# Kernel tuning notes

Measured on AMD Instinct MI355X. Metric: run time of the kernel, lower is better.

Reference implementation:

```python
import jax, jax.numpy as jnp
import numpy as np

L, H, NH, B, S = 6, 768, 12, 4, 1024
D = H // NH
SCALE = 1.0 / np.sqrt(D)
EPS = 1e-5


def setup_inputs() -> dict:
    key = jax.random.key(0)
    ks = jax.random.split(key, 20)
    std = np.sqrt(2.0 / (5.0 * H)).astype(np.float32)
    w = lambda k, shape: (jax.random.normal(k, shape, jnp.float32) * std)
    x = jax.random.normal(ks[0], (B, S, H), jnp.float32)
    lengths = jnp.array([1024, 896, 768, 640])  # no fully-masked rows
    pad_mask = jnp.arange(S)[None, :] >= lengths[:, None]  # True = padding
    inp = {
        "x": x,
        "pad_mask": pad_mask,
        "Wq": w(ks[1], (L, H, H)), "bq": jnp.zeros((L, H), jnp.float32),
        "Wk": w(ks[2], (L, H, H)), "bk": w(ks[3], (L, H)) * 0.1,
        "Wv": w(ks[4], (L, H, H)), "bv": w(ks[5], (L, H)) * 0.1,
        "Wo": w(ks[6], (L, H, H)), "bo": jnp.zeros((L, H), jnp.float32),
        "ln1_g": jnp.ones((L, H), jnp.float32), "ln1_b": jnp.zeros((L, H), jnp.float32),
        "ln2_g": jnp.ones((L, H), jnp.float32), "ln2_b": jnp.zeros((L, H), jnp.float32),
        "W1": w(ks[7], (L, 8 * H, H)), "b1": jnp.zeros((L, 8 * H), jnp.float32),
        "W2": w(ks[8], (L, H, 4 * H)), "b2": jnp.zeros((L, H), jnp.float32),
        "out_g": jnp.ones((H,), jnp.float32), "out_b": jnp.zeros((H,), jnp.float32),
    }
    return inp


def _ln(x, g, b):
    m = jnp.mean(x, axis=-1, keepdims=True)
    v = jnp.mean(jnp.square(x - m), axis=-1, keepdims=True)
    return (x - m) * jax.lax.rsqrt(v + EPS) * g + b


def _encoder(x, pad_mask, params):
    def layer(x, p):
        (Wq, bq, Wk, bk, Wv, bv, Wo, bo, g1, be1, g2, be2, W1, b1, W2, b2) = p
        Bz, Sl, Hd = x.shape
        xn = _ln(x, g1, be1)
        q = (xn @ Wq.T + bq).reshape(Bz, Sl, NH, D)
        k = (xn @ Wk.T + bk).reshape(Bz, Sl, NH, D)
        v = (xn @ Wv.T + bv).reshape(Bz, Sl, NH, D)
        scores = jnp.einsum('bqhd,bkhd->bhqk', q, k) * SCALE
        scores = jnp.where(pad_mask[:, None, None, :], -jnp.inf, scores)
        probs = jax.nn.softmax(scores, axis=-1)
        av = jnp.einsum('bhqk,bkhd->bqhd', probs, v).reshape(Bz, Sl, Hd)
        x = x + (av @ Wo.T + bo)
        xn = _ln(x, g2, be2)
        h = xn @ W1.T + b1
        u, gate = jnp.split(h, 2, axis=-1)
        x = x + (u * jax.nn.gelu(gate, approximate=False)) @ W2.T + b2
        return x, None

    x, _ = jax.lax.scan(layer, x, params)
    return x


def reference(x, pad_mask, Wq, bq, Wk, bk, Wv, bv, Wo, bo,
              ln1_g, ln1_b, ln2_g, ln2_b, W1, b1, W2, b2, out_g, out_b):
    params = (Wq, bq, Wk, bk, Wv, bv, Wo, bo,
              ln1_g, ln1_b, ln2_g, ln2_b, W1, b1, W2, b2)
    x = _encoder(x, pad_mask, params)
    return _ln(x, out_g, out_b)
```

## Files before the change

kernel.cpp:

```cpp
#include <hip/hip_runtime.h>

typedef unsigned short u16;
typedef __bf16 bf16x8 __attribute__((ext_vector_type(8)));
typedef unsigned short us8 __attribute__((ext_vector_type(8)));
typedef unsigned short us4 __attribute__((ext_vector_type(4)));
typedef float f32x4 __attribute__((ext_vector_type(4)));

typedef __attribute__((address_space(3))) unsigned int as3_uint;
typedef const __attribute__((address_space(1))) unsigned int as1_cuint;

__device__ __forceinline__ u16 f2bf(float f) {
    unsigned u = __float_as_uint(f);
    u += 0x7FFFu + ((u >> 16) & 1u);
    return (u16)(u >> 16);
}
__device__ __forceinline__ float bf2f(u16 h) {
    return __uint_as_float(((unsigned)h) << 16);
}
__device__ __forceinline__ bf16x8 ld8(const u16* p) {
    return __builtin_bit_cast(bf16x8, *(const us8*)p);
}
#define MFMA16(a, b, c) __builtin_amdgcn_mfma_f32_16x16x32_bf16(a, b, c, 0, 0, 0)

__device__ __forceinline__ void glds16(const void* g, void* l) {
    __builtin_amdgcn_global_load_lds((as1_cuint*)g, (as3_uint*)l, 16, 0, 0);
}

__global__ void detect_k(const unsigned* __restrict__ pm, int* __restrict__ len4) {
    __shared__ int isbool;
    const int t = threadIdx.x;
    if (t == 0) isbool = 0;
    __syncthreads();
    unsigned orv = pm[t] | pm[256 + t] | pm[512 + t] | pm[768 + t];
    if (orv & 0xFFFFFF00u) atomicOr(&isbool, 1);
    __syncthreads();
    const int w = t >> 6, l = t & 63;
    int cnt = 0;
    if (isbool) {
        const unsigned char* p8 = (const unsigned char*)pm;
        for (int i = l; i < 1024; i += 64) cnt += (p8[w * 1024 + i] == 0) ? 1 : 0;
    } else {
        for (int i = l; i < 1024; i += 64) cnt += (pm[w * 1024 + i] == 0u) ? 1 : 0;
    }
#pragma unroll
    for (int m = 1; m < 64; m <<= 1) cnt += __shfl_xor(cnt, m);
    if (l == 0) {
        int c = cnt;
        if (c < 1) c = 1;
        if (c > 1024) c = 1024;
        len4[w] = c;
    }
}

__global__ __launch_bounds__(256) void conv_k(
    const float* __restrict__ Wq, const float* __restrict__ Wk,
    const float* __restrict__ Wv, const float* __restrict__ Wo,
    const float* __restrict__ W1, const float* __restrict__ W2,
    const float* __restrict__ bq, const float* __restrict__ bk,
    const float* __restrict__ bv,
    u16* __restrict__ wqkvo, u16* __restrict__ w1b, u16* __restrict__ w2b,
    float* __restrict__ bqkv, int lyr) {
    const int idx = blockIdx.x * 256 + threadIdx.x;
    const size_t e = (size_t)idx * 4;
    const float* src;
    u16* dst;
    if (e < 2359296u) {
        int which = (int)(e / 589824u);
        size_t off = e % 589824u;
        const float* m = (which == 0) ? Wq : (which == 1) ? Wk : (which == 2) ? Wv : Wo;
        src = m + (size_t)lyr * 589824u + off;
        dst = wqkvo + e;
    } else if (e < 7077888u) {
        size_t off = e - 2359296u;
        src = W1 + (size_t)lyr * 4718592u + off;
        dst = w1b + off;
    } else {
        size_t off = e - 7077888u;
        src = W2 + (size_t)lyr * 2359296u + off;
        dst = w2b + off;
    }
    float4 v = *(const float4*)src;
    us4 o;
    o[0] = f2bf(v.x); o[1] = f2bf(v.y); o[2] = f2bf(v.z); o[3] = f2bf(v.w);
    *(us4*)dst = o;
    if (idx < 2304) {
        float bb = (idx < 768) ? bq[lyr * 768 + idx]
                 : (idx < 1536) ? bk[lyr * 768 + idx - 768]
                                : bv[lyr * 768 + idx - 1536];
        bqkv[idx] = bb;
    }
}

template <int OUTF>
__global__ __launch_bounds__(256) void ln_k(const float* __restrict__ x,
                                            const float* __restrict__ gm,
                                            const float* __restrict__ bt,
                                            void* __restrict__ outp) {
    const int w = threadIdx.x >> 6, l = threadIdx.x & 63;
    const int row = blockIdx.x * 4 + w;
    const float4* xr = (const float4*)(x + (size_t)row * 768);
    float4 v[3];
    float s = 0.f, ss = 0.f;
#pragma unroll
    for (int i = 0; i < 3; ++i) {
        v[i] = xr[i * 64 + l];
        s += v[i].x + v[i].y + v[i].z + v[i].w;
        ss += v[i].x * v[i].x + v[i].y * v[i].y + v[i].z * v[i].z + v[i].w * v[i].w;
    }
#pragma unroll
    for (int m = 1; m < 64; m <<= 1) {
        s += __shfl_xor(s, m);
        ss += __shfl_xor(ss, m);
    }
    const float mean = s * (1.f / 768.f);
    float var = ss * (1.f / 768.f) - mean * mean;
    var = fmaxf(var, 0.f);
    const float rs = rsqrtf(var + 1e-5f);
    const float4* g4 = (const float4*)gm;
    const float4* b4 = (const float4*)bt;
#pragma unroll
    for (int i = 0; i < 3; ++i) {
        float4 gg = g4[i * 64 + l], bb = b4[i * 64 + l];
        float o0 = (v[i].x - mean) * rs * gg.x + bb.x;
        float o1 = (v[i].y - mean) * rs * gg.y + bb.y;
        float o2 = (v[i].z - mean) * rs * gg.z + bb.z;
        float o3 = (v[i].w - mean) * rs * gg.w + bb.w;
        if (OUTF) {
            ((float4*)outp)[(size_t)row * 192 + i * 64 + l] = make_float4(o0, o1, o2, o3);
        } else {
            us4 pk;
            pk[0] = f2bf(o0); pk[1] = f2bf(o1); pk[2] = f2bf(o2); pk[3] = f2bf(o3);
            ((us4*)outp)[(size_t)row * 192 + i * 64 + l] = pk;
        }
    }
}

template <int VAR>
__global__ __launch_bounds__(512, 2) void gemm256_k(
    const u16* __restrict__ A, const u16* __restrict__ W,
    const float* __restrict__ bias, u16* __restrict__ outp, int ldout) {
    __shared__ __align__(16) u16 lds[2][4][8192];
    const int tid = threadIdx.x;
    const int w = tid >> 6, l = tid & 63, ax = l & 15, gx = l >> 4;
    const int wr = w >> 2, wc = w & 3;
    const int nwg = gridDim.x;
    const int bid = blockIdx.x;
    const int swz = (bid & 7) * (nwg >> 3) + (bid >> 3);
    const int nb = swz >> 4, mb = swz & 15;
    const int m0 = mb * 256;
    const int K = 768;

    const int row0 = tid >> 2, cc0 = (tid & 3) ^ ((row0 >> 1) & 3);
    const int row1 = 128 + row0, cc1 = (tid & 3) ^ ((row1 >> 1) & 3);
    const size_t goA0 = (size_t)row0 * K + cc0 * 8;
    const size_t goA1 = (size_t)row1 * K + cc1 * 8;
    const u16* Ab = A + (size_t)m0 * K;
    const u16* Bb0;
    const u16* Bb1;
    if constexpr (VAR == 0) {
        Bb0 = W + (size_t)(nb * 256) * K;
        Bb1 = Bb0;
    } else {
        Bb0 = W + (size_t)(nb * 128) * K;
        Bb1 = W + (size_t)(3072 + nb * 128 - 128) * K;
    }

    auto stage = [&](int u, int kt) {
        const int kh = u & 1;
        const size_t koff = (size_t)kt * 64 + kh * 32;
        u16* d = (u16*)&lds[kt & 1][u][0];
        if (u < 2) {
            glds16(Ab + goA0 + koff, d + tid * 8);
            glds16(Ab + goA1 + koff, d + (512 + tid) * 8);
        } else {
            glds16(Bb0 + goA0 + koff, d + tid * 8);
            glds16(Bb1 + goA1 + koff, d + (512 + tid) * 8);
        }
    };

    bf16x8 rav[4], rbv[4];
    f32x4 acc[8][4] = {};

    auto phase = [&](int buf, int q, int kh, int readB, int vm, int su, int skt) {
        if (vm == 8) asm volatile("s_waitcnt vmcnt(8)" ::: "memory");
        else if (vm == 4) asm volatile("s_waitcnt vmcnt(4)" ::: "memory");
        else if (vm == 0) asm volatile("s_waitcnt vmcnt(0)" ::: "memory");
        __builtin_amdgcn_s_barrier();
        if (readB) {
#pragma unroll
            for (int j = 0; j < 4; ++j) {
                int row = (VAR == 0) ? (wc * 64 + j * 16 + ax)
                                     : ((j >> 1) * 128 + wc * 32 + (j & 1) * 16 + ax);
                rbv[j] = ld8(&lds[buf][2 + kh][row * 32 + ((gx ^ ((row >> 1) & 3)) * 8)]);
            }
        }
#pragma unroll
        for (int mf = 0; mf < 4; ++mf) {
            int row = wr * 128 + q * 64 + mf * 16 + ax;
            rav[mf] = ld8(&lds[buf][kh][row * 32 + ((gx ^ ((row >> 1) & 3)) * 8)]);
        }
        if (su >= 0) stage(su, skt);
        asm volatile("s_waitcnt lgkmcnt(0)" ::: "memory");
        __builtin_amdgcn_sched_barrier(0);
        __builtin_amdgcn_s_setprio(1);
#pragma unroll
        for (int mf = 0; mf < 4; ++mf)
#pragma unroll
            for (int j = 0; j < 4; ++j)
                acc[q * 4 + mf][j] = MFMA16(rav[mf], rbv[j], acc[q * 4 + mf][j]);
        __builtin_amdgcn_s_setprio(0);
    };

    stage(0, 0); stage(2, 0); stage(1, 0); stage(3, 0); stage(0, 1); stage(2, 1);

#pragma unroll 1
    for (int t = 0; t < 5; ++t) {
        const int O = 2 * t + 1, E2 = 2 * t + 2, O2 = 2 * t + 3;
        phase(0, 0, 0, 1, 8, 1, O);
        phase(0, 1, 0, 0, -1, 3, O);
        phase(0, 0, 1, 1, 8, 0, E2);
        phase(0, 1, 1, 0, -1, 2, E2);
        phase(1, 0, 0, 1, 8, 1, E2);
        phase(1, 1, 0, 0, -1, 3, E2);
        phase(1, 0, 1, 1, 8, 0, O2);
        phase(1, 1, 1, 0, -1, 2, O2);
    }
    phase(0, 0, 0, 1, 8, 1, 11);
    phase(0, 1, 0, 0, -1, 3, 11);
    phase(0, 0, 1, 1, 8, -1, 0);
    phase(0, 1, 1, 0, -1, -1, 0);
    phase(1, 0, 0, 1, 4, -1, 0);
    phase(1, 1, 0, 0, -1, -1, 0);
    phase(1, 0, 1, 1, 0, -1, 0);
    phase(1, 1, 1, 0, -1, -1, 0);

    const int rowb = m0 + wr * 128;
    if constexpr (VAR == 0) {
#pragma unroll
        for (int j = 0; j < 4; ++j) {
            const int col = nb * 256 + wc * 64 + j * 16 + ax;
            const float bn = bias[col];
#pragma unroll
            for (int am = 0; am < 8; ++am) {
                const int rb_ = rowb + am * 16 + 4 * gx;
#pragma unroll
                for (int r = 0; r < 4; ++r)
                    outp[(size_t)(rb_ + r) * ldout + col] = f2bf(acc[am][j][r] + bn);
            }
        }
    } else {
#pragma unroll
        for (int nf = 0; nf < 2; ++nf) {
            const int col = nb * 128 + wc * 32 + nf * 16 + ax;
            const float bu_ = bias[col], bg_ = bias[3072 + col];
#pragma unroll
            for (int am = 0; am < 8; ++am) {
                const int rb_ = rowb + am * 16 + 4 * gx;
#pragma unroll
                for (int r = 0; r < 4; ++r) {
                    float uu = acc[am][nf][r] + bu_;
                    float gg = acc[am][2 + nf][r] + bg_;
                    float gel = 0.5f * gg * (1.f + erff(gg * 0.70710678118f));
                    outp[(size_t)(rb_ + r) * ldout + col] = f2bf(uu * gel);
                }
            }
        }
    }
}

template <int EPI>
__global__ __launch_bounds__(256) void gemm_k(
    const u16* __restrict__ A, const u16* __restrict__ W,
    const float* __restrict__ bias, const float* __restrict__ resid,
    void* __restrict__ outp, int N, int K) {
    __shared__ __align__(16) u16 As[2][128 * 64];
    __shared__ __align__(16) u16 Bs[2][128 * 64];
    const int tid = threadIdx.x;
    const int w = tid >> 6, l = tid & 63, a = l & 15, g = l >> 4;
    const int wr = w >> 1, wc = w & 1;
    const int m0 = blockIdx.y * 128, n0 = blockIdx.x * 128;
    f32x4 acc[4][4] = {};
    const int nk = K >> 6;

    auto stage = [&](int kt, int buf) {
        const int k0 = kt * 64;
#pragma unroll
        for (int i = 0; i < 4; ++i) {
            int c = i * 256 + tid;
            int row = c >> 3, cc = c & 7, c8 = cc ^ (row & 7);
            glds16(A + (size_t)(m0 + row) * K + k0 + c8 * 8, &As[buf][c * 8]);
        }
#pragma unroll
        for (int i = 0; i < 4; ++i) {
            int c = i * 256 + tid;
            int row = c >> 3, cc = c & 7, c8 = cc ^ (row & 7);
            glds16(W + (size_t)(n0 + row) * K + k0 + c8 * 8, &Bs[buf][c * 8]);
        }
    };

    stage(0, 0);
    int cur = 0;
    for (int kt = 0; kt < nk; ++kt) {
        if (kt + 1 < nk) {
            stage(kt + 1, cur ^ 1);
            __builtin_amdgcn_sched_barrier(0);
            asm volatile("s_waitcnt vmcnt(8)" ::: "memory");
        } else {
            __builtin_amdgcn_sched_barrier(0);
            asm volatile("s_waitcnt vmcnt(0)" ::: "memory");
        }
        __builtin_amdgcn_s_barrier();
#pragma unroll
        for (int ks = 0; ks < 2; ++ks) {
            bf16x8 af[4], bv_[4];
#pragma unroll
            for (int m = 0; m < 4; ++m) {
                int row = wr * 64 + m * 16 + a;
                af[m] = ld8(&As[cur][row * 64 + (((ks * 4 + g) ^ (a & 7)) * 8)]);
            }
#pragma unroll
            for (int n = 0; n < 4; ++n) {
                int row = wc * 64 + n * 16 + a;
                bv_[n] = ld8(&Bs[cur][row * 64 + (((ks * 4 + g) ^ (a & 7)) * 8)]);
            }
#pragma unroll
            for (int m = 0; m < 4; ++m)
#pragma unroll
                for (int n = 0; n < 4; ++n)
                    acc[m][n] = MFMA16(af[m], bv_[n], acc[m][n]);
        }
        __builtin_amdgcn_s_barrier();
        cur ^= 1;
    }
    u16* outu = (u16*)outp;
    float* outf = (float*)outp;
    const int row0 = m0 + wr * 64, col0 = n0 + wc * 64;
#pragma unroll
    for (int n = 0; n < 4; ++n) {
        const int col = col0 + n * 16 + a;
        const float bn = bias[col];
#pragma unroll
        for (int m = 0; m < 4; ++m) {
            const int rb = row0 + m * 16 + 4 * g;
#pragma unroll
            for (int r = 0; r < 4; ++r) {
                const size_t off = (size_t)(rb + r) * N + col;
                float vv = acc[m][n][r] + bn;
                if constexpr (EPI == 0) {
                    outu[off] = f2bf(vv);
                } else {
                    outf[off] = vv + resid[off];
                }
            }
        }
    }
}

__global__ __launch_bounds__(256) void attn_k(const u16* __restrict__ qkv,
                                              u16* __restrict__ av,
                                              const int* __restrict__ len4) {
    __shared__ __align__(16) u16 Ks[64 * 64];
    __shared__ __align__(16) u16 Vt[64 * 64];
    __shared__ __align__(16) u16 Ps[4][16 * 64];
    const int tid = threadIdx.x;
    const int w = tid >> 6, l = tid & 63, a = l & 15, g = l >> 4;
    const int qb = blockIdx.x, h = blockIdx.y, b = blockIdx.z;
    const size_t rowQ = (size_t)(b * 1024 + qb * 64 + w * 16 + a);
    const u16* qp = qkv + rowQ * 2304 + h * 64;
    bf16x8 qf[2];
    qf[0] = __builtin_bit_cast(bf16x8, *(const us8*)(qp + g * 8));
    qf[1] = __builtin_bit_cast(bf16x8, *(const us8*)(qp + 32 + g * 8));
    f32x4 O[4] = {};
    float m_r[4], l_r[4];
#pragma unroll
    for (int r = 0; r < 4; ++r) { m_r[r] = -1e30f; l_r[r] = 0.f; }
    const int length = len4[b];
    const int nkt = (length + 63) >> 6;
    for (int kt = 0; kt < nkt; ++kt) {
        __syncthreads();
#pragma unroll
        for (int i = 0; i < 2; ++i) {
            int c = i * 256 + tid;
            int row = c >> 3, cc = c & 7, c8 = cc ^ (row & 7);
            glds16(qkv + (size_t)(b * 1024 + kt * 64 + row) * 2304 + 768 + h * 64 + c8 * 8,
                   &Ks[c * 8]);
        }
        {
            const int d = l;
            const u16* vcol = qkv + (size_t)(b * 1024 + kt * 64) * 2304 + 1536 + h * 64 + d;
#pragma unroll
            for (int i = 0; i < 2; ++i) {
                int kkc = w + 4 * i;
                us8 vv;
#pragma unroll
                for (int j = 0; j < 8; ++j) vv[j] = vcol[(size_t)(kkc * 8 + j) * 2304];
                int cc = kkc ^ (d & 7);
                *(us8*)&Vt[d * 64 + cc * 8] = vv;
            }
        }
        __syncthreads();
        f32x4 s[4] = {};
#pragma unroll
        for (int ks = 0; ks < 2; ++ks) {
#pragma unroll
            for (int f = 0; f < 4; ++f) {
                int row = f * 16 + a;
                bf16x8 kf = ld8(&Ks[row * 64 + (((ks * 4 + g) ^ (a & 7)) * 8)]);
                s[f] = MFMA16(qf[ks], kf, s[f]);
            }
        }
        float mloc[4] = {-1e30f, -1e30f, -1e30f, -1e30f};
#pragma unroll
        for (int f = 0; f < 4; ++f) {
            int kkg = kt * 64 + f * 16 + a;
            bool valid = kkg < length;
#pragma unroll
            for (int r = 0; r < 4; ++r) {
                float v = valid ? s[f][r] * 0.125f : -1e30f;
                s[f][r] = v;
                mloc[r] = fmaxf(mloc[r], v);
            }
        }
#pragma unroll
        for (int r = 0; r < 4; ++r) {
#pragma unroll
            for (int m = 1; m < 16; m <<= 1)
                mloc[r] = fmaxf(mloc[r], __shfl_xor(mloc[r], m));
        }
        float al[4], ps[4];
#pragma unroll
        for (int r = 0; r < 4; ++r) {
            float nm = fmaxf(m_r[r], mloc[r]);
            al[r] = __expf(m_r[r] - nm);
            m_r[r] = nm;
            ps[r] = 0.f;
        }
#pragma unroll
        for (int f = 0; f < 4; ++f)
#pragma unroll
            for (int r = 0; r < 4; ++r) {
                float p = __expf(s[f][r] - m_r[r]);
                s[f][r] = p;
                ps[r] += p;
            }
#pragma unroll
        for (int r = 0; r < 4; ++r) {
#pragma unroll
            for (int m = 1; m < 16; m <<= 1) ps[r] += __shfl_xor(ps[r], m);
            l_r[r] = l_r[r] * al[r] + ps[r];
        }
#pragma unroll
        for (int df = 0; df < 4; ++df)
#pragma unroll
            for (int r = 0; r < 4; ++r) O[df][r] *= al[r];
#pragma unroll
        for (int f = 0; f < 4; ++f)
#pragma unroll
            for (int r = 0; r < 4; ++r) {
                int prow = 4 * g + r;
                int cc = (2 * f + (a >> 3)) ^ (prow & 7);
                Ps[w][prow * 64 + cc * 8 + (a & 7)] = f2bf(s[f][r]);
            }
        asm volatile("s_waitcnt lgkmcnt(0)" ::: "memory");
        __builtin_amdgcn_sched_barrier(0);
#pragma unroll
        for (int ks = 0; ks < 2; ++ks) {
            bf16x8 pf = ld8(&Ps[w][a * 64 + (((ks * 4 + g) ^ (a & 7)) * 8)]);
#pragma unroll
            for (int df = 0; df < 4; ++df) {
                int vrow = df * 16 + a;
                bf16x8 vf = ld8(&Vt[vrow * 64 + (((ks * 4 + g) ^ (a & 7)) * 8)]);
                O[df] = MFMA16(pf, vf, O[df]);
            }
        }
    }
#pragma unroll
    for (int df = 0; df < 4; ++df) {
        int col = h * 64 + df * 16 + a;
#pragma unroll
        for (int r = 0; r < 4; ++r) {
            int row = b * 1024 + qb * 64 + w * 16 + 4 * g + r;
            av[(size_t)row * 768 + col] = f2bf(O[df][r] / l_r[r]);
        }
    }
}

extern "C" void kernel_launch(void* const* d_in, const int* in_sizes, int n_in,
                              void* d_out, int out_size, void* d_ws, size_t ws_size,
                              hipStream_t stream) {
    const float* x_in = (const float*)d_in[0];
    const unsigned* pm = (const unsigned*)d_in[1];
    const float* Wq = (const float*)d_in[2];
    const float* bq = (const float*)d_in[3];
    const float* Wk = (const float*)d_in[4];
    const float* bk = (const float*)d_in[5];
    const float* Wv = (const float*)d_in[6];
    const float* bv = (const float*)d_in[7];
    const float* Wo = (const float*)d_in[8];
    const float* bo = (const float*)d_in[9];
    const float* g1 = (const float*)d_in[10];
    const float* be1 = (const float*)d_in[11];
    const float* g2 = (const float*)d_in[12];
    const float* be2 = (const float*)d_in[13];
    const float* W1 = (const float*)d_in[14];
    const float* b1 = (const float*)d_in[15];
    const float* W2 = (const float*)d_in[16];
    const float* b2 = (const float*)d_in[17];
    const float* og = (const float*)d_in[18];
    const float* ob = (const float*)d_in[19];

    char* ws = (char*)d_ws;
    u16* wqkvo = (u16*)(ws + 0);
    u16* w1b   = (u16*)(ws + 4718592);
    u16* w2b   = (u16*)(ws + 14155776);
    float* bqkv = (float*)(ws + 18874368);
    int* len4  = (int*)(ws + 18883584);
    float* xbuf = (float*)(ws + 18883840);
    u16* xn    = (u16*)(ws + 31466752);
    u16* qkv   = (u16*)(ws + 37758208);
    u16* avb   = (u16*)(ws + 56632576);
    u16* ub    = (u16*)(ws + 62924032);

    detect_k<<<1, 256, 0, stream>>>(pm, len4);
    for (int l = 0; l < 6; ++l) {
        conv_k<<<9216, 256, 0, stream>>>(Wq, Wk, Wv, Wo, W1, W2, bq, bk, bv,
                                         wqkvo, w1b, w2b, bqkv, l);
        const float* xcur = (l == 0) ? x_in : xbuf;
        ln_k<0><<<1024, 256, 0, stream>>>(xcur, g1 + l * 768, be1 + l * 768, xn);
        gemm256_k<0><<<144, 512, 0, stream>>>(xn, wqkvo, bqkv, qkv, 2304);
        attn_k<<<dim3(16, 12, 4), 256, 0, stream>>>(qkv, avb, len4);
        gemm_k<1><<<dim3(6, 32), 256, 0, stream>>>(avb, wqkvo + 3 * 589824, bo + l * 768,
                                                   xcur, xbuf, 768, 768);
        ln_k<0><<<1024, 256, 0, stream>>>(xbuf, g2 + l * 768, be2 + l * 768, xn);
        gemm256_k<1><<<384, 512, 0, stream>>>(xn, w1b, b1 + l * 6144, ub, 3072);
        gemm_k<1><<<dim3(6, 32), 256, 0, stream>>>(ub, w2b, b2 + l * 768, xbuf,
                                                   xbuf, 768, 3072);
    }
    ln_k<1><<<1024, 256, 0, stream>>>(xbuf, og, ob, d_out);
}
```

Measured before the change: 1.337 ms.

## Retile GEMMs for CU coverage, chain FFN1 tiles, and emit transposed V

Moves the 256x256 GEMM body into a templated device function. The QKV projection now uses 256x192 tiles over 192 blocks, and the FFN1 GEMM runs 256 blocks that each compute a 256-wide tile followed by a 128-wide tile, with the next tile's loads prefetched in the tail of the first. The QKV epilogue writes V transposed into a separate buffer, so attention loads V with contiguous vector reads instead of strided gathers. The 128x128 GEMMs move to 512 threads with 8 waves, which gives each wave fewer accumulators. Risks include the vT buffer aliasing the ub buffer, smaller per-wave MFMA work, and the extra complexity of the chained-tile pipeline.

```diff
diff --git a/kernel.cpp b/kernel.cpp
--- a/kernel.cpp
+++ b/kernel.cpp
@@ -135,62 +135,57 @@
     }
 }
 
-template <int VAR>
-__global__ __launch_bounds__(512, 2) void gemm256_k(
-    const u16* __restrict__ A, const u16* __restrict__ W,
-    const float* __restrict__ bias, u16* __restrict__ outp, int ldout) {
-    __shared__ __align__(16) u16 lds[2][4][8192];
+template <int VAR, int NF, int CHAIN, int PRO>
+__device__ __forceinline__ void g256_body(
+    const u16* __restrict__ Ab, const u16* __restrict__ Bb0,
+    const u16* __restrict__ Bb1,
+    const u16* __restrict__ AbN, const u16* __restrict__ Bb0N,
+    const u16* __restrict__ Bb1N,
+    const float* __restrict__ bias, u16* __restrict__ outp,
+    u16* __restrict__ vT, int ldout, int ncol0, int m0,
+    u16 (&lds)[2][4][8192]) {
     const int tid = threadIdx.x;
     const int w = tid >> 6, l = tid & 63, ax = l & 15, gx = l >> 4;
     const int wr = w >> 2, wc = w & 3;
-    const int nwg = gridDim.x;
-    const int bid = blockIdx.x;
-    const int swz = (bid & 7) * (nwg >> 3) + (bid >> 3);
-    const int nb = swz >> 4, mb = swz & 15;
-    const int m0 = mb * 256;
     const int K = 768;
 
     const int row0 = tid >> 2, cc0 = (tid & 3) ^ ((row0 >> 1) & 3);
     const int row1 = 128 + row0, cc1 = (tid & 3) ^ ((row1 >> 1) & 3);
     const size_t goA0 = (size_t)row0 * K + cc0 * 8;
     const size_t goA1 = (size_t)row1 * K + cc1 * 8;
-    const u16* Ab = A + (size_t)m0 * K;
-    const u16* Bb0;
-    const u16* Bb1;
-    if constexpr (VAR == 0) {
-        Bb0 = W + (size_t)(nb * 256) * K;
-        Bb1 = Bb0;
-    } else {
-        Bb0 = W + (size_t)(nb * 128) * K;
-        Bb1 = W + (size_t)(3072 + nb * 128 - 128) * K;
-    }
-
-    auto stage = [&](int u, int kt) {
+
+    auto stage = [&](int u, int kt, int nxt) {
         const int kh = u & 1;
         const size_t koff = (size_t)kt * 64 + kh * 32;
         u16* d = (u16*)&lds[kt & 1][u][0];
+        const u16* A_ = nxt ? AbN : Ab;
+        const u16* B0_ = nxt ? Bb0N : Bb0;
+        const u16* B1_ = nxt ? Bb1N : Bb1;
         if (u < 2) {
-            glds16(Ab + goA0 + koff, d + tid * 8);
-            glds16(Ab + goA1 + koff, d + (512 + tid) * 8);
+            glds16(A_ + goA0 + koff, d + tid * 8);
+            glds16(A_ + goA1 + koff, d + (512 + tid) * 8);
         } else {
-            glds16(Bb0 + goA0 + koff, d + tid * 8);
-            glds16(Bb1 + goA1 + koff, d + (512 + tid) * 8);
+            glds16(B0_ + goA0 + koff, d + tid * 8);
+            glds16(B1_ + goA1 + koff, d + (512 + tid) * 8);
         }
     };
 
-    bf16x8 rav[4], rbv[4];
-    f32x4 acc[8][4] = {};
-
-    auto phase = [&](int buf, int q, int kh, int readB, int vm, int su, int skt) {
+    bf16x8 rav[4], rbv[NF];
+    f32x4 acc[8][NF] = {};
+
+    auto phase = [&](int buf, int q, int kh, int readB, int vm, int su, int skt,
+                     int nxt) {
         if (vm == 8) asm volatile("s_waitcnt vmcnt(8)" ::: "memory");
         else if (vm == 4) asm volatile("s_waitcnt vmcnt(4)" ::: "memory");
         else if (vm == 0) asm volatile("s_waitcnt vmcnt(0)" ::: "memory");
         __builtin_amdgcn_s_barrier();
         if (readB) {
 #pragma unroll
-            for (int j = 0; j < 4; ++j) {
-                int row = (VAR == 0) ? (wc * 64 + j * 16 + ax)
-                                     : ((j >> 1) * 128 + wc * 32 + (j & 1) * 16 + ax);
+            for (int j = 0; j < NF; ++j) {
+                int row;
+                if (VAR == 0) row = wc * (16 * NF) + j * 16 + ax;
+                else row = ((j >= NF / 2) ? 128 : 0) + wc * (8 * NF) +
+                           (j % (NF / 2)) * 16 + ax;
                 rbv[j] = ld8(&lds[buf][2 + kh][row * 32 + ((gx ^ ((row >> 1) & 3)) * 8)]);
             }
         }
@@ -199,67 +194,99 @@
             int row = wr * 128 + q * 64 + mf * 16 + ax;
             rav[mf] = ld8(&lds[buf][kh][row * 32 + ((gx ^ ((row >> 1) & 3)) * 8)]);
         }
-        if (su >= 0) stage(su, skt);
+        if (su >= 0) stage(su, skt, nxt);
         asm volatile("s_waitcnt lgkmcnt(0)" ::: "memory");
         __builtin_amdgcn_sched_barrier(0);
         __builtin_amdgcn_s_setprio(1);
 #pragma unroll
         for (int mf = 0; mf < 4; ++mf)
 #pragma unroll
-            for (int j = 0; j < 4; ++j)
+            for (int j = 0; j < NF; ++j)
                 acc[q * 4 + mf][j] = MFMA16(rav[mf], rbv[j], acc[q * 4 + mf][j]);
         __builtin_amdgcn_s_setprio(0);
     };
 
-    stage(0, 0); stage(2, 0); stage(1, 0); stage(3, 0); stage(0, 1); stage(2, 1);
+    if (PRO) {
+        stage(0, 0, 0); stage(2, 0, 0); stage(1, 0, 0);
+        stage(3, 0, 0); stage(0, 1, 0); stage(2, 1, 0);
+    }
 
 #pragma unroll 1
     for (int t = 0; t < 5; ++t) {
         const int O = 2 * t + 1, E2 = 2 * t + 2, O2 = 2 * t + 3;
-        phase(0, 0, 0, 1, 8, 1, O);
-        phase(0, 1, 0, 0, -1, 3, O);
-        phase(0, 0, 1, 1, 8, 0, E2);
-        phase(0, 1, 1, 0, -1, 2, E2);
-        phase(1, 0, 0, 1, 8, 1, E2);
-        phase(1, 1, 0, 0, -1, 3, E2);
-        phase(1, 0, 1, 1, 8, 0, O2);
-        phase(1, 1, 1, 0, -1, 2, O2);
-    }
-    phase(0, 0, 0, 1, 8, 1, 11);
-    phase(0, 1, 0, 0, -1, 3, 11);
-    phase(0, 0, 1, 1, 8, -1, 0);
-    phase(0, 1, 1, 0, -1, -1, 0);
-    phase(1, 0, 0, 1, 4, -1, 0);
-    phase(1, 1, 0, 0, -1, -1, 0);
-    phase(1, 0, 1, 1, 0, -1, 0);
-    phase(1, 1, 1, 0, -1, -1, 0);
+        phase(0, 0, 0, 1, 8, 1, O, 0);
+        phase(0, 1, 0, 0, -1, 3, O, 0);
+        phase(0, 0, 1, 1, 8, 0, E2, 0);
+        phase(0, 1, 1, 0, -1, 2, E2, 0);
+        phase(1, 0, 0, 1, 8, 1, E2, 0);
+        phase(1, 1, 0, 0, -1, 3, E2, 0);
+        phase(1, 0, 1, 1, 8, 0, O2, 0);
+        phase(1, 1, 1, 0, -1, 2, O2, 0);
+    }
+    if (CHAIN) {
+        phase(0, 0, 0, 1, 8, 1, 11, 0);
+        phase(0, 1, 0, 0, -1, 3, 11, 0);
+        phase(0, 0, 1, 1, 8, 0, 0, 1);
+        phase(0, 1, 1, 0, -1, 2, 0, 1);
+        phase(1, 0, 0, 1, 8, 1, 0, 1);
+        phase(1, 1, 0, 0, -1, 3, 0, 1);
+        phase(1, 0, 1, 1, 8, 0, 1, 1);
+        phase(1, 1, 1, 0, -1, 2, 1, 1);
+    } else {
+        phase(0, 0, 0, 1, 8, 1, 11, 0);
+        phase(0, 1, 0, 0, -1, 3, 11, 0);
+        phase(0, 0, 1, 1, 8, -1, 0, 0);
+        phase(0, 1, 1, 0, -1, -1, 0, 0);
+        phase(1, 0, 0, 1, 4, -1, 0, 0);
+        phase(1, 1, 0, 0, -1, -1, 0, 0);
+        phase(1, 0, 1, 1, 0, -1, 0, 0);
+        phase(1, 1, 1, 0, -1, -1, 0, 0);
+    }
 
     const int rowb = m0 + wr * 128;
-    if constexpr (VAR == 0) {
-#pragma unroll
-        for (int j = 0; j < 4; ++j) {
-            const int col = nb * 256 + wc * 64 + j * 16 + ax;
-            const float bn = bias[col];
+    if (VAR == 0) {
+        if (ncol0 >= 1536) {
+#pragma unroll
+            for (int j = 0; j < NF; ++j) {
+                const int col = ncol0 + wc * (16 * NF) + j * 16 + ax;
+                const float bn = bias[col];
+                u16* vcol = vT + (size_t)(col - 1536) * 4096;
+#pragma unroll
+                for (int am = 0; am < 8; ++am) {
+                    const int rb_ = rowb + am * 16 + 4 * gx;
+                    us4 pk;
+#pragma unroll
+                    for (int r = 0; r < 4; ++r) pk[r] = f2bf(acc[am][j][r] + bn);
+                    *(us4*)(vcol + rb_) = pk;
+                }
+            }
+        } else {
+#pragma unroll
+            for (int j = 0; j < NF; ++j) {
+                const int col = ncol0 + wc * (16 * NF) + j * 16 + ax;
+                const float bn = bias[col];
+#pragma unroll
+                for (int am = 0; am < 8; ++am) {
+                    const int rb_ = rowb + am * 16 + 4 * gx;
+#pragma unroll
+                    for (int r = 0; r < 4; ++r)
+                        outp[(size_t)(rb_ + r) * ldout + col] = f2bf(acc[am][j][r] + bn);
+                }
+            }
+        }
+    } else {
+        const int P = NF / 2;
+#pragma unroll
+        for (int nf = 0; nf < NF / 2; ++nf) {
+            const int col = ncol0 + wc * (16 * P) + nf * 16 + ax;
+            const float bu_ = bias[col], bg_ = bias[3072 + col];
 #pragma unroll
             for (int am = 0; am < 8; ++am) {
                 const int rb_ = rowb + am * 16 + 4 * gx;
 #pragma unroll
-                for (int r = 0; r < 4; ++r)
-                    outp[(size_t)(rb_ + r) * ldout + col] = f2bf(acc[am][j][r] + bn);
-            }
-        }
-    } else {
-#pragma unroll
-        for (int nf = 0; nf < 2; ++nf) {
-            const int col = nb * 128 + wc * 32 + nf * 16 + ax;
-            const float bu_ = bias[col], bg_ = bias[3072 + col];
-#pragma unroll
-            for (int am = 0; am < 8; ++am) {
-                const int rb_ = rowb + am * 16 + 4 * gx;
-#pragma unroll
                 for (int r = 0; r < 4; ++r) {
                     float uu = acc[am][nf][r] + bu_;
-                    float gg = acc[am][2 + nf][r] + bg_;
+                    float gg = acc[am][P + nf][r] + bg_;
                     float gel = 0.5f * gg * (1.f + erff(gg * 0.70710678118f));
                     outp[(size_t)(rb_ + r) * ldout + col] = f2bf(uu * gel);
                 }
@@ -268,8 +295,42 @@
     }
 }
 
+__global__ __launch_bounds__(512, 2) void qkv256_k(
+    const u16* __restrict__ A, const u16* __restrict__ W,
+    const float* __restrict__ bias, u16* __restrict__ outp,
+    u16* __restrict__ vT) {
+    __shared__ __align__(16) u16 lds[2][4][8192];
+    const int bid = blockIdx.x;
+    const int swz = (bid & 7) * 24 + (bid >> 3);
+    const int nb = swz >> 4, mb = swz & 15;
+    const int m0 = mb * 256;
+    const u16* Ab = A + (size_t)m0 * 768;
+    const u16* Bb0 = W + (size_t)(nb * 192) * 768;
+    g256_body<0, 3, 0, 1>(Ab, Bb0, Bb0, nullptr, nullptr, nullptr,
+                          bias, outp, vT, 2304, nb * 192, m0, lds);
+}
+
+__global__ __launch_bounds__(512, 2) void ffn1_k(
+    const u16* __restrict__ A, const u16* __restrict__ W,
+    const float* __restrict__ bias, u16* __restrict__ outp) {
+    __shared__ __align__(16) u16 lds[2][4][8192];
+    const int bid = blockIdx.x;
+    const int swz = (bid & 7) * 32 + (bid >> 3);
+    const int nb = swz >> 4, mb = swz & 15;
+    const int m0 = mb * 256;
+    const u16* Ab = A + (size_t)m0 * 768;
+    const u16* Bb0 = W + (size_t)(nb * 128) * 768;
+    const u16* Bb1 = W + (size_t)(3072 + nb * 128 - 128) * 768;
+    const u16* Bb0h = W + (size_t)(2048 + nb * 64) * 768;
+    const u16* Bb1h = W + (size_t)(5120 + nb * 64 - 128) * 768;
+    g256_body<1, 4, 1, 1>(Ab, Bb0, Bb1, Ab, Bb0h, Bb1h,
+                          bias, outp, nullptr, 3072, nb * 128, m0, lds);
+    g256_body<1, 2, 0, 0>(Ab, Bb0h, Bb1h, nullptr, nullptr, nullptr,
+                          bias, outp, nullptr, 3072, 2048 + nb * 64, m0, lds);
+}
+
 template <int EPI>
-__global__ __launch_bounds__(256) void gemm_k(
+__global__ __launch_bounds__(512) void gemm_k(
     const u16* __restrict__ A, const u16* __restrict__ W,
     const float* __restrict__ bias, const float* __restrict__ resid,
     void* __restrict__ outp, int N, int K) {
@@ -277,22 +338,22 @@
     __shared__ __align__(16) u16 Bs[2][128 * 64];
     const int tid = threadIdx.x;
     const int w = tid >> 6, l = tid & 63, a = l & 15, g = l >> 4;
-    const int wr = w >> 1, wc = w & 1;
+    const int wr = w >> 2, wc = w & 3;
     const int m0 = blockIdx.y * 128, n0 = blockIdx.x * 128;
-    f32x4 acc[4][4] = {};
+    f32x4 acc[4][2] = {};
     const int nk = K >> 6;
 
     auto stage = [&](int kt, int buf) {
         const int k0 = kt * 64;
 #pragma unroll
-        for (int i = 0; i < 4; ++i) {
-            int c = i * 256 + tid;
+        for (int i = 0; i < 2; ++i) {
+            int c = i * 512 + tid;
             int row = c >> 3, cc = c & 7, c8 = cc ^ (row & 7);
             glds16(A + (size_t)(m0 + row) * K + k0 + c8 * 8, &As[buf][c * 8]);
         }
 #pragma unroll
-        for (int i = 0; i < 4; ++i) {
-            int c = i * 256 + tid;
+        for (int i = 0; i < 2; ++i) {
+            int c = i * 512 + tid;
             int row = c >> 3, cc = c & 7, c8 = cc ^ (row & 7);
             glds16(W + (size_t)(n0 + row) * K + k0 + c8 * 8, &Bs[buf][c * 8]);
         }
@@ -304,7 +365,7 @@
         if (kt + 1 < nk) {
             stage(kt + 1, cur ^ 1);
             __builtin_amdgcn_sched_barrier(0);
-            asm volatile("s_waitcnt vmcnt(8)" ::: "memory");
+            asm volatile("s_waitcnt vmcnt(4)" ::: "memory");
         } else {
             __builtin_amdgcn_sched_barrier(0);
             asm volatile("s_waitcnt vmcnt(0)" ::: "memory");
@@ -312,21 +373,21 @@
         __builtin_amdgcn_s_barrier();
 #pragma unroll
         for (int ks = 0; ks < 2; ++ks) {
-            bf16x8 af[4], bv_[4];
+            bf16x8 af[4], bv_[2];
 #pragma unroll
             for (int m = 0; m < 4; ++m) {
                 int row = wr * 64 + m * 16 + a;
                 af[m] = ld8(&As[cur][row * 64 + (((ks * 4 + g) ^ (a & 7)) * 8)]);
             }
 #pragma unroll
-            for (int n = 0; n < 4; ++n) {
-                int row = wc * 64 + n * 16 + a;
+            for (int n = 0; n < 2; ++n) {
+                int row = wc * 32 + n * 16 + a;
                 bv_[n] = ld8(&Bs[cur][row * 64 + (((ks * 4 + g) ^ (a & 7)) * 8)]);
             }
 #pragma unroll
             for (int m = 0; m < 4; ++m)
 #pragma unroll
-                for (int n = 0; n < 4; ++n)
+                for (int n = 0; n < 2; ++n)
                     acc[m][n] = MFMA16(af[m], bv_[n], acc[m][n]);
         }
         __builtin_amdgcn_s_barrier();
@@ -334,9 +395,9 @@
     }
     u16* outu = (u16*)outp;
     float* outf = (float*)outp;
-    const int row0 = m0 + wr * 64, col0 = n0 + wc * 64;
-#pragma unroll
-    for (int n = 0; n < 4; ++n) {
+    const int row0 = m0 + wr * 64, col0 = n0 + wc * 32;
+#pragma unroll
+    for (int n = 0; n < 2; ++n) {
         const int col = col0 + n * 16 + a;
         const float bn = bias[col];
 #pragma unroll
@@ -357,6 +418,7 @@
 }
 
 __global__ __launch_bounds__(256) void attn_k(const u16* __restrict__ qkv,
+                                              const u16* __restrict__ vT,
                                               u16* __restrict__ av,
                                               const int* __restrict__ len4) {
     __shared__ __align__(16) u16 Ks[64 * 64];
@@ -387,13 +449,11 @@
         }
         {
             const int d = l;
-            const u16* vcol = qkv + (size_t)(b * 1024 + kt * 64) * 2304 + 1536 + h * 64 + d;
+            const u16* vrow = vT + (size_t)(h * 64 + d) * 4096 + b * 1024 + kt * 64;
 #pragma unroll
             for (int i = 0; i < 2; ++i) {
                 int kkc = w + 4 * i;
-                us8 vv;
-#pragma unroll
-                for (int j = 0; j < 8; ++j) vv[j] = vcol[(size_t)(kkc * 8 + j) * 2304];
+                us8 vv = *(const us8*)(vrow + kkc * 8);
                 int cc = kkc ^ (d & 7);
                 *(us8*)&Vt[d * 64 + cc * 8] = vv;
             }
@@ -520,6 +580,7 @@
     u16* qkv   = (u16*)(ws + 37758208);
     u16* avb   = (u16*)(ws + 56632576);
     u16* ub    = (u16*)(ws + 62924032);
+    u16* vT    = (u16*)(ws + 62924032);
 
     detect_k<<<1, 256, 0, stream>>>(pm, len4);
     for (int l = 0; l < 6; ++l) {
@@ -527,13 +588,13 @@
                                          wqkvo, w1b, w2b, bqkv, l);
         const float* xcur = (l == 0) ? x_in : xbuf;
         ln_k<0><<<1024, 256, 0, stream>>>(xcur, g1 + l * 768, be1 + l * 768, xn);
-        gemm256_k<0><<<144, 512, 0, stream>>>(xn, wqkvo, bqkv, qkv, 2304);
-        attn_k<<<dim3(16, 12, 4), 256, 0, stream>>>(qkv, avb, len4);
-        gemm_k<1><<<dim3(6, 32), 256, 0, stream>>>(avb, wqkvo + 3 * 589824, bo + l * 768,
+        qkv256_k<<<192, 512, 0, stream>>>(xn, wqkvo, bqkv, qkv, vT);
+        attn_k<<<dim3(16, 12, 4), 256, 0, stream>>>(qkv, vT, avb, len4);
+        gemm_k<1><<<dim3(6, 32), 512, 0, stream>>>(avb, wqkvo + 3 * 589824, bo + l * 768,
                                                    xcur, xbuf, 768, 768);
         ln_k<0><<<1024, 256, 0, stream>>>(xbuf, g2 + l * 768, be2 + l * 768, xn);
-        gemm256_k<1><<<384, 512, 0, stream>>>(xn, w1b, b1 + l * 6144, ub, 3072);
-        gemm_k<1><<<dim3(6, 32), 256, 0, stream>>>(ub, w2b, b2 + l * 768, xbuf,
+        ffn1_k<<<256, 512, 0, stream>>>(xn, w1b, b1 + l * 6144, ub);
+        gemm_k<1><<<dim3(6, 32), 512, 0, stream>>>(ub, w2b, b2 + l * 768, xbuf,
                                                    xbuf, 768, 3072);
     }
     ln_k<1><<<1024, 256, 0, stream>>>(xbuf, og, ob, d_out);
```

Measured after the change: 1.256 ms. -6.1%, faster.
